# Optimization experiments

Measured on AMD Instinct MI355X. Metric: run time of the kernel, lower is better.

## Reference

```python
import jax, jax.numpy as jnp
import numpy as np

N_EVENTS = 16
N_SAMPLES = 2 ** 15  # 32768


def fft_shift(stems, shift_samples):
    """Fractionally shift each atom in time via frequency-domain phase rotation.
    stems: (B, E, N) float32; shift_samples: (B, E) float32 in [0, N].
    """
    n = stems.shape[-1]
    freqs = jnp.fft.rfftfreq(n).astype(jnp.float32)  # (n//2+1,) cycles/sample
    theta = 2.0 * jnp.pi * freqs[None, None, :] * shift_samples[..., None]  # (B,E,F)
    phase = jnp.cos(theta) - 1j * jnp.sin(theta)  # exp(-i*theta)
    spec = jnp.fft.rfft(stems, axis=-1)
    return jnp.fft.irfft(spec * phase, n=n, axis=-1)


def setup_inputs() -> dict:
    key = jax.random.key(0)
    k1, k2, k3, k4 = jax.random.split(key, 4)
    B = 64
    time_latent = jax.random.normal(k1, (B, N_EVENTS, 128), dtype=jnp.float32)
    stems = jax.random.normal(k2, (B, N_EVENTS, N_SAMPLES), dtype=jnp.float32)
    targets = jax.random.normal(k3, (B, 1, N_SAMPLES), dtype=jnp.float32)
    W_pos = jax.random.normal(k4, (1, 128), dtype=jnp.float32) * 0.1
    b_pos = jnp.zeros((1,), dtype=jnp.float32)
    return {"time_latent": time_latent, "stems": stems, "targets": targets,
            "W_pos": W_pos, "b_pos": b_pos}


def reference(time_latent, stems, targets, W_pos, b_pos):
    # to_pos: Linear(128 -> 1), then sigmoid -> fractional positions in [0,1]
    pos = jax.nn.sigmoid(jnp.einsum('bed,od->beo', time_latent, W_pos) + b_pos)
    pos = pos.reshape(-1, N_EVENTS)  # (B, E)
    # schedule_atoms: place each stem at fractional offset pos * n_samples, sum events
    shifted = fft_shift(stems, pos * N_SAMPLES)  # (B, E, N)
    scheduled = jnp.sum(shifted, axis=1, keepdims=True)  # (B, 1, N), same shape as targets
    return scheduled
```

## Files before the change

### kernel.cpp

```cpp
#include <hip/hip_runtime.h>
#include <math.h>

#define NS      32768
#define M       16384
#define NEV     16
#define NB      64
#define T2      1024

__device__ __forceinline__ int ldsIdx(int i) { return i + (i >> 5) + (i >> 10); }
#define LDS_ELEMS (M + M / 32 + M / 1024)

__device__ __forceinline__ float2 cmul(float2 a, float2 b) {
    return make_float2(a.x * b.x - a.y * b.y, a.x * b.y + a.y * b.x);
}

__device__ __forceinline__ int rev4_14(int i) {
    int r = 0;
#pragma unroll
    for (int d = 0; d < 7; ++d) { r = (r << 2) | (i & 3); i >>= 2; }
    return r;
}

__device__ __forceinline__ float2 shift_phase(int k, int si, float sf) {
    unsigned ksi = ((unsigned)k * (unsigned)si) & (unsigned)(NS - 1);
    float total = (float)ksi + (float)k * sf;
    float f = total * (1.0f / (float)NS);
    f -= floorf(f);
    float ang = -6.28318530717958647692f * f;
    float sv, cv;
    __sincosf(ang, &sv, &cv);
    return make_float2(cv, sv);
}

__device__ __forceinline__ float2 wNS(int k) {
    float ang = (float)k * (-6.28318530717958647692f / (float)NS);
    float sv, cv;
    __sincosf(ang, &sv, &cv);
    return make_float2(cv, sv);
}

__device__ __constant__ float R16C[4] = {1.0f, 0.92387953251128675613f,
                                         0.70710678118654752440f, 0.38268343236508977173f};
__device__ __constant__ float R16S[4] = {0.0f, 0.38268343236508977173f,
                                         0.70710678118654752440f, 0.92387953251128675613f};

__device__ __constant__ float C32[16] = {
    1.0f, 0.98078528040323044913f, 0.92387953251128675613f, 0.83146961230254523708f,
    0.70710678118654752440f, 0.55557023301960222474f, 0.38268343236508977173f,
    0.19509032201612826785f, 0.0f, -0.19509032201612826785f, -0.38268343236508977173f,
    -0.55557023301960222474f, -0.70710678118654752440f, -0.83146961230254523708f,
    -0.92387953251128675613f, -0.98078528040323044913f};
__device__ __constant__ float S32[16] = {
    0.0f, 0.19509032201612826785f, 0.38268343236508977173f, 0.55557023301960222474f,
    0.70710678118654752440f, 0.83146961230254523708f, 0.92387953251128675613f,
    0.98078528040323044913f, 1.0f, 0.98078528040323044913f, 0.92387953251128675613f,
    0.83146961230254523708f, 0.70710678118654752440f, 0.55557023301960222474f,
    0.38268343236508977173f, 0.19509032201612826785f};

template <int SIGN>
__device__ __forceinline__ void btf4(float2* a) {
    float2 a0 = a[0], a1 = a[1], a2 = a[2], a3 = a[3];
    float2 u0 = make_float2(a0.x + a2.x, a0.y + a2.y);
    float2 u1 = make_float2(a0.x - a2.x, a0.y - a2.y);
    float2 u2 = make_float2(a1.x + a3.x, a1.y + a3.y);
    float2 u3 = make_float2(a1.x - a3.x, a1.y - a3.y);
    a[0] = make_float2(u0.x + u2.x, u0.y + u2.y);
    a[2] = make_float2(u0.x - u2.x, u0.y - u2.y);
    if (SIGN < 0) {
        a[1] = make_float2(u1.x + u3.y, u1.y - u3.x);
        a[3] = make_float2(u1.x - u3.y, u1.y + u3.x);
    } else {
        a[1] = make_float2(u1.x - u3.y, u1.y + u3.x);
        a[3] = make_float2(u1.x + u3.y, u1.y - u3.x);
    }
}

template <int SIGN>
__device__ __forceinline__ void load_stage0_scatter(const float4* __restrict__ src,
                                                    float2* lds, int tid) {
    const int R = rev4_14(2 * tid);
    float2 g0[4], g1[4], g2[4], g3[4];
#pragma unroll
    for (int it = 0; it < 8; ++it) {
        float4 v = src[tid + (it << 10)];
        int l = it >> 1;
        if ((it & 1) == 0) { g0[l] = make_float2(v.x, v.y); g1[l] = make_float2(v.z, v.w); }
        else               { g2[l] = make_float2(v.x, v.y); g3[l] = make_float2(v.z, v.w); }
    }
    btf4<SIGN>(g0); btf4<SIGN>(g1); btf4<SIGN>(g2); btf4<SIGN>(g3);
#pragma unroll
    for (int l = 0; l < 4; ++l) {
        lds[ldsIdx(R + l)]               = g0[l];
        lds[ldsIdx(R + 4096 + l)]        = g1[l];
        lds[ldsIdx(R + 8 + l)]           = g2[l];
        lds[ldsIdx(R + 8 + 4096 + l)]    = g3[l];
    }
}

template <int SIGN>
__device__ void fft_pairs(float2* lds, int tid) {
    const float TP = (SIGN < 0) ? -6.28318530717958647692f
                                :  6.28318530717958647692f;
#pragma unroll
    for (int tp = 0; tp < 3; ++tp) {
        const int t = 2 * tp + 1;
        const int q = 1 << (2 * t);
        const int j = tid & (q - 1);
        const int base = ((tid >> (2 * t)) << (2 * t + 4)) + j;
        float2 x[16];
#pragma unroll
        for (int l = 0; l < 16; ++l) x[l] = lds[ldsIdx(base + l * q)];

        float sv, cv;
        __sincosf(TP * (float)j / (float)(16 * q), &sv, &cv);
        float2 ww = make_float2(cv, sv);
        float2 s2 = cmul(ww, ww);
        float2 w1 = cmul(s2, s2);
        float2 w2 = cmul(w1, w1);
        float2 w3 = cmul(w2, w1);

#pragma unroll
        for (int m = 0; m < 4; ++m) {
            float2 a0 = x[4 * m], a1 = x[4 * m + 1], a2 = x[4 * m + 2], a3 = x[4 * m + 3];
            a1 = cmul(a1, w1); a2 = cmul(a2, w2); a3 = cmul(a3, w3);
            float2 u0 = make_float2(a0.x + a2.x, a0.y + a2.y);
            float2 u1 = make_float2(a0.x - a2.x, a0.y - a2.y);
            float2 u2 = make_float2(a1.x + a3.x, a1.y + a3.y);
            float2 u3 = make_float2(a1.x - a3.x, a1.y - a3.y);
            x[4 * m]     = make_float2(u0.x + u2.x, u0.y + u2.y);
            x[4 * m + 2] = make_float2(u0.x - u2.x, u0.y - u2.y);
            if (SIGN < 0) {
                x[4 * m + 1] = make_float2(u1.x + u3.y, u1.y - u3.x);
                x[4 * m + 3] = make_float2(u1.x - u3.y, u1.y + u3.x);
            } else {
                x[4 * m + 1] = make_float2(u1.x - u3.y, u1.y + u3.x);
                x[4 * m + 3] = make_float2(u1.x + u3.y, u1.y - u3.x);
            }
        }

#pragma unroll
        for (int n = 0; n < 4; ++n) {
            float2 a0 = x[n], a1 = x[n + 4], a2 = x[n + 8], a3 = x[n + 12];
            {
                float2 r = make_float2(R16C[n], (SIGN < 0) ? -R16S[n] : R16S[n]);
                float2 wp = (n > 0) ? cmul(ww, r) : ww;
                float2 wp2 = cmul(wp, wp);
                float2 wp3 = cmul(wp2, wp);
                a1 = cmul(a1, wp);
                a2 = cmul(a2, wp2);
                a3 = cmul(a3, wp3);
            }
            float2 u0 = make_float2(a0.x + a2.x, a0.y + a2.y);
            float2 u1 = make_float2(a0.x - a2.x, a0.y - a2.y);
            float2 u2 = make_float2(a1.x + a3.x, a1.y + a3.y);
            float2 u3 = make_float2(a1.x - a3.x, a1.y - a3.y);
            x[n]      = make_float2(u0.x + u2.x, u0.y + u2.y);
            x[n + 8]  = make_float2(u0.x - u2.x, u0.y - u2.y);
            if (SIGN < 0) {
                x[n + 4]  = make_float2(u1.x + u3.y, u1.y - u3.x);
                x[n + 12] = make_float2(u1.x - u3.y, u1.y + u3.x);
            } else {
                x[n + 4]  = make_float2(u1.x - u3.y, u1.y + u3.x);
                x[n + 12] = make_float2(u1.x + u3.y, u1.y - u3.x);
            }
        }
#pragma unroll
        for (int l = 0; l < 16; ++l) lds[ldsIdx(base + l * q)] = x[l];
        __syncthreads();
    }
}

__device__ __forceinline__ void zpair(float2 a, float2 bb, float2 w,
                                      float2* z1, float2* z2) {
    float2 E1 = make_float2(0.5f * (a.x + bb.x), 0.5f * (a.y - bb.y));
    float2 D1 = make_float2(0.5f * (a.x - bb.x), 0.5f * (a.y + bb.y));
    float2 O1 = cmul(make_float2(w.x, -w.y), D1);
    *z1 = make_float2(E1.x - O1.y, E1.y + O1.x);
    float2 D2 = make_float2(-D1.x, D1.y);
    float2 O2p = cmul(w, D2);
    *z2 = make_float2(E1.x + O2p.y, -E1.y - O2p.x);
}

__global__ __launch_bounds__(T2, 4) void fft_phase_kernel(float* __restrict__ stems,
                                                          const float* __restrict__ tl,
                                                          const float* __restrict__ W,
                                                          const float* __restrict__ bp) {
    __shared__ float2 lds[LDS_ELEMS];
    __shared__ float sh_shift;
    const int tid = threadIdx.x;
    const int row = blockIdx.x;
    float* rowp = stems + (size_t)row * NS;

    if (tid < 64) {
        const float* trow = tl + (size_t)row * 128;
        float p = trow[tid] * W[tid] + trow[tid + 64] * W[tid + 64];
#pragma unroll
        for (int off = 32; off > 0; off >>= 1) p += __shfl_down(p, off);
        if (tid == 0) {
            float x = p + bp[0];
            sh_shift = (1.0f / (1.0f + expf(-x))) * (float)NS;
        }
    }

    load_stage0_scatter<-1>((const float4*)rowp, lds, tid);
    __syncthreads();
    fft_pairs<-1>(lds, tid);

    const float s = sh_shift;
    const int si = (int)floorf(s);
    const float sf = s - (float)si;
    float2* spec = (float2*)rowp;

    float msv, mcv;
    __sincosf(-3.14159265358979323846f * sf, &msv, &mcv);
    float2 phM = make_float2(mcv, msv);
    if (si & 1) { phM.x = -phM.x; phM.y = -phM.y; }

    const float2 ph0 = shift_phase(tid, si, sf);
    const float2 w0  = wNS(tid);
    const float2 q1  = shift_phase(1024, si, sf);
    const float2 q2  = cmul(q1, q1);
    const float2 q3  = cmul(q2, q1);
    const float2 q4  = cmul(q2, q2);
    float2 phb = ph0;
#pragma unroll
    for (int t = 0; t < 8; ++t) {
        int k = tid + (t << 10);
        float2 ph;
        switch (t & 3) {
            case 0:  ph = phb; break;
            case 1:  ph = cmul(phb, q1); break;
            case 2:  ph = cmul(phb, q2); break;
            default: ph = cmul(phb, q3); break;
        }
        if (k == 0) {
            float2 z0 = lds[ldsIdx(0)];
            float X0 = z0.x + z0.y;
            float XM = z0.x - z0.y;
            float Nq = XM * phM.x;
            spec[0] = make_float2(0.5f * (X0 + Nq), 0.5f * (X0 - Nq));
            float2 Zh = lds[ldsIdx(M / 2)];
            float2 Xh = make_float2(Zh.x, -Zh.y);
            float2 ph_h = shift_phase(M / 2, si, sf);
            float2 Ah = cmul(Xh, ph_h);
            spec[M / 2] = make_float2(Ah.x, -Ah.y);
        } else {
            float2 Zk = lds[ldsIdx(k)];
            float2 Zr = lds[ldsIdx(M - k)];
            float2 E = make_float2(0.5f * (Zk.x + Zr.x), 0.5f * (Zk.y - Zr.y));
            float2 O = make_float2(0.5f * (Zk.y + Zr.y), -0.5f * (Zk.x - Zr.x));
            float2 w = cmul(w0, make_float2(C32[t], -S32[t]));
            float2 wo = cmul(w, O);
            float2 Xk = make_float2(E.x + wo.x, E.y + wo.y);
            float2 Xm = make_float2(E.x - wo.x, wo.y - E.y);
            float2 Ak = cmul(Xk, ph);
            float2 phm = cmul(phM, make_float2(ph.x, -ph.y));
            float2 Am = cmul(Xm, phm);
            float2 z1, z2;
            zpair(Ak, Am, w, &z1, &z2);
            spec[k] = z1;
            spec[M - k] = z2;
        }
        if ((t & 3) == 3) phb = cmul(phb, q4);
    }
}

__global__ __launch_bounds__(256) void reduce_kernel(const float4* __restrict__ stems,
                                                     float4* __restrict__ out) {
    int gid = blockIdx.x * 256 + threadIdx.x;
    int b = gid >> 13;
    int i = gid & (NS / 4 - 1);
    const float4* base = stems + (size_t)b * NEV * (NS / 4) + i;
    float4 s = base[0];
#pragma unroll
    for (int e = 1; e < NEV; ++e) {
        float4 v = base[(size_t)e * (NS / 4)];
        s.x += v.x; s.y += v.y; s.z += v.z; s.w += v.w;
    }
    out[gid] = s;
}

__global__ __launch_bounds__(T2, 4) void inv_kernel(float* __restrict__ out) {
    __shared__ float2 lds[LDS_ELEMS];
    const int tid = threadIdx.x;
    const int b = blockIdx.x;
    float* rowp = out + (size_t)b * NS;

    load_stage0_scatter<1>((const float4*)rowp, lds, tid);
    __syncthreads();
    fft_pairs<1>(lds, tid);

    const float invM = 1.0f / (float)M;
    float4* dst = (float4*)rowp;
#pragma unroll
    for (int it = 0; it < (NS / 4) / T2; ++it) {
        int i = tid + it * T2;
        float2 z0 = lds[ldsIdx(2 * i)];
        float2 z1 = lds[ldsIdx(2 * i + 1)];
        dst[i] = make_float4(z0.x * invM, z0.y * invM, z1.x * invM, z1.y * invM);
    }
}

extern "C" void kernel_launch(void* const* d_in, const int* in_sizes, int n_in,
                              void* d_out, int out_size, void* d_ws, size_t ws_size,
                              hipStream_t stream) {
    const float* time_latent = (const float*)d_in[0];
    float* stems = (float*)d_in[1];
    const float* W_pos = (const float*)d_in[3];
    const float* b_pos = (const float*)d_in[4];
    float* out = (float*)d_out;

    fft_phase_kernel<<<NB * NEV, T2, 0, stream>>>(stems, time_latent, W_pos, b_pos);
    reduce_kernel<<<(NB * NS / 4) / 256, 256, 0, stream>>>((const float4*)stems,
                                                           (float4*)out);
    inv_kernel<<<NB, T2, 0, stream>>>(out);
}
```

Before: 284.7 us.

## Accumulate four events' shifted spectra per block before writing partials

Each block now runs forward FFTs and phase shifts for four events in sequence and keeps the summed spectrum in registers. It writes one partial spectrum per group of four instead of one per event, and the reduce kernel sums only four partials. This cuts global write and reduce read traffic by four times. In exchange the grid shrinks to a quarter as many blocks, each doing serial work with extra accumulator registers, which may reduce latency hiding. If the workspace is too small it falls back to writing partials into the stems buffer, which could overwrite rows other blocks have not read yet.

```diff
diff --git a/kernel.cpp b/kernel.cpp
--- a/kernel.cpp
+++ b/kernel.cpp
@@ -6,6 +6,8 @@
 #define NEV     16
 #define NB      64
 #define T2      1024
+#define EPB     4
+#define NGRP    (NEV / EPB)
 
 __device__ __forceinline__ int ldsIdx(int i) { return i + (i >> 5) + (i >> 10); }
 #define LDS_ELEMS (M + M / 32 + M / 1024)
@@ -181,100 +183,138 @@
     *z2 = make_float2(E1.x + O2p.y, -E1.y - O2p.x);
 }
 
-__global__ __launch_bounds__(T2, 4) void fft_phase_kernel(float* __restrict__ stems,
-                                                          const float* __restrict__ tl,
-                                                          const float* __restrict__ W,
-                                                          const float* __restrict__ bp) {
+__global__ __launch_bounds__(T2, 4) void fft_phase_acc(const float* __restrict__ stems,
+                                                       float* __restrict__ zpart,
+                                                       const float* __restrict__ tl,
+                                                       const float* __restrict__ W,
+                                                       const float* __restrict__ bp) {
     __shared__ float2 lds[LDS_ELEMS];
-    __shared__ float sh_shift;
+    __shared__ float sh_shift[EPB];
     const int tid = threadIdx.x;
-    const int row = blockIdx.x;
-    float* rowp = stems + (size_t)row * NS;
-
-    if (tid < 64) {
-        const float* trow = tl + (size_t)row * 128;
-        float p = trow[tid] * W[tid] + trow[tid + 64] * W[tid + 64];
+    const int b = blockIdx.x >> 2;
+    const int g = blockIdx.x & 3;
+    const int rowbase = b * NEV + g * EPB;
+
+    if (tid < EPB * 64) {
+        const int w = tid >> 6, lane = tid & 63;
+        const float* trow = tl + (size_t)(rowbase + w) * 128;
+        float p = trow[lane] * W[lane] + trow[lane + 64] * W[lane + 64];
 #pragma unroll
         for (int off = 32; off > 0; off >>= 1) p += __shfl_down(p, off);
-        if (tid == 0) {
+        if (lane == 0) {
             float x = p + bp[0];
-            sh_shift = (1.0f / (1.0f + expf(-x))) * (float)NS;
-        }
-    }
-
-    load_stage0_scatter<-1>((const float4*)rowp, lds, tid);
-    __syncthreads();
-    fft_pairs<-1>(lds, tid);
-
-    const float s = sh_shift;
-    const int si = (int)floorf(s);
-    const float sf = s - (float)si;
-    float2* spec = (float2*)rowp;
-
-    float msv, mcv;
-    __sincosf(-3.14159265358979323846f * sf, &msv, &mcv);
-    float2 phM = make_float2(mcv, msv);
-    if (si & 1) { phM.x = -phM.x; phM.y = -phM.y; }
-
-    const float2 ph0 = shift_phase(tid, si, sf);
-    const float2 w0  = wNS(tid);
-    const float2 q1  = shift_phase(1024, si, sf);
-    const float2 q2  = cmul(q1, q1);
-    const float2 q3  = cmul(q2, q1);
-    const float2 q4  = cmul(q2, q2);
-    float2 phb = ph0;
+            sh_shift[w] = (1.0f / (1.0f + expf(-x))) * (float)NS;
+        }
+    }
+
+    float2 accK[8], accR[8];
+#pragma unroll
+    for (int t = 0; t < 8; ++t) {
+        accK[t] = make_float2(0.f, 0.f);
+        accR[t] = make_float2(0.f, 0.f);
+    }
+    const float2 w0 = wNS(tid);
+
+    for (int ee = 0; ee < EPB; ++ee) {
+        const float* rowp = stems + (size_t)(rowbase + ee) * NS;
+        load_stage0_scatter<-1>((const float4*)rowp, lds, tid);
+        __syncthreads();
+        fft_pairs<-1>(lds, tid);
+
+        const float s = sh_shift[ee];
+        const int si = (int)floorf(s);
+        const float sf = s - (float)si;
+
+        float msv, mcv;
+        __sincosf(-3.14159265358979323846f * sf, &msv, &mcv);
+        float2 phM = make_float2(mcv, msv);
+        if (si & 1) { phM.x = -phM.x; phM.y = -phM.y; }
+
+        const float2 ph0 = shift_phase(tid, si, sf);
+        const float2 q1  = shift_phase(1024, si, sf);
+        const float2 q2  = cmul(q1, q1);
+        const float2 q3  = cmul(q2, q1);
+        const float2 q4  = cmul(q2, q2);
+        float2 phb = ph0;
+#pragma unroll
+        for (int t = 0; t < 8; ++t) {
+            int k = tid + (t << 10);
+            float2 ph;
+            switch (t & 3) {
+                case 0:  ph = phb; break;
+                case 1:  ph = cmul(phb, q1); break;
+                case 2:  ph = cmul(phb, q2); break;
+                default: ph = cmul(phb, q3); break;
+            }
+            if (k == 0) {
+                float2 z0 = lds[ldsIdx(0)];
+                float X0 = z0.x + z0.y;
+                float XM = z0.x - z0.y;
+                float Nq = XM * phM.x;
+                accK[0].x += 0.5f * (X0 + Nq);
+                accK[0].y += 0.5f * (X0 - Nq);
+                float2 Zh = lds[ldsIdx(M / 2)];
+                float2 Xh = make_float2(Zh.x, -Zh.y);
+                float2 ph_h = shift_phase(M / 2, si, sf);
+                float2 Ah = cmul(Xh, ph_h);
+                accR[0].x += Ah.x;
+                accR[0].y += -Ah.y;
+            } else {
+                float2 Zk = lds[ldsIdx(k)];
+                float2 Zr = lds[ldsIdx(M - k)];
+                float2 E = make_float2(0.5f * (Zk.x + Zr.x), 0.5f * (Zk.y - Zr.y));
+                float2 O = make_float2(0.5f * (Zk.y + Zr.y), -0.5f * (Zk.x - Zr.x));
+                float2 w = cmul(w0, make_float2(C32[t], -S32[t]));
+                float2 wo = cmul(w, O);
+                float2 Xk = make_float2(E.x + wo.x, E.y + wo.y);
+                float2 Xm = make_float2(E.x - wo.x, wo.y - E.y);
+                float2 Ak = cmul(Xk, ph);
+                float2 phm = cmul(phM, make_float2(ph.x, -ph.y));
+                float2 Am = cmul(Xm, phm);
+                float2 z1, z2;
+                zpair(Ak, Am, w, &z1, &z2);
+                accK[t].x += z1.x; accK[t].y += z1.y;
+                accR[t].x += z2.x; accR[t].y += z2.y;
+            }
+            if ((t & 3) == 3) phb = cmul(phb, q4);
+        }
+        __syncthreads();
+    }
+
 #pragma unroll
     for (int t = 0; t < 8; ++t) {
         int k = tid + (t << 10);
-        float2 ph;
-        switch (t & 3) {
-            case 0:  ph = phb; break;
-            case 1:  ph = cmul(phb, q1); break;
-            case 2:  ph = cmul(phb, q2); break;
-            default: ph = cmul(phb, q3); break;
-        }
         if (k == 0) {
-            float2 z0 = lds[ldsIdx(0)];
-            float X0 = z0.x + z0.y;
-            float XM = z0.x - z0.y;
-            float Nq = XM * phM.x;
-            spec[0] = make_float2(0.5f * (X0 + Nq), 0.5f * (X0 - Nq));
-            float2 Zh = lds[ldsIdx(M / 2)];
-            float2 Xh = make_float2(Zh.x, -Zh.y);
-            float2 ph_h = shift_phase(M / 2, si, sf);
-            float2 Ah = cmul(Xh, ph_h);
-            spec[M / 2] = make_float2(Ah.x, -Ah.y);
+            lds[ldsIdx(0)]     = accK[0];
+            lds[ldsIdx(M / 2)] = accR[0];
         } else {
-            float2 Zk = lds[ldsIdx(k)];
-            float2 Zr = lds[ldsIdx(M - k)];
-            float2 E = make_float2(0.5f * (Zk.x + Zr.x), 0.5f * (Zk.y - Zr.y));
-            float2 O = make_float2(0.5f * (Zk.y + Zr.y), -0.5f * (Zk.x - Zr.x));
-            float2 w = cmul(w0, make_float2(C32[t], -S32[t]));
-            float2 wo = cmul(w, O);
-            float2 Xk = make_float2(E.x + wo.x, E.y + wo.y);
-            float2 Xm = make_float2(E.x - wo.x, wo.y - E.y);
-            float2 Ak = cmul(Xk, ph);
-            float2 phm = cmul(phM, make_float2(ph.x, -ph.y));
-            float2 Am = cmul(Xm, phm);
-            float2 z1, z2;
-            zpair(Ak, Am, w, &z1, &z2);
-            spec[k] = z1;
-            spec[M - k] = z2;
-        }
-        if ((t & 3) == 3) phb = cmul(phb, q4);
-    }
-}
-
-__global__ __launch_bounds__(256) void reduce_kernel(const float4* __restrict__ stems,
-                                                     float4* __restrict__ out) {
+            lds[ldsIdx(k)]     = accK[t];
+            lds[ldsIdx(M - k)] = accR[t];
+        }
+    }
+    __syncthreads();
+
+    float4* dst = (float4*)(zpart + (size_t)(g * NB + b) * NS);
+#pragma unroll
+    for (int it = 0; it < (NS / 4) / T2; ++it) {
+        int i = tid + it * T2;
+        float2 z0 = lds[ldsIdx(2 * i)];
+        float2 z1 = lds[ldsIdx(2 * i + 1)];
+        dst[i] = make_float4(z0.x, z0.y, z1.x, z1.y);
+    }
+}
+
+__global__ __launch_bounds__(256) void reduce4_kernel(const float4* __restrict__ zpart,
+                                                      float4* __restrict__ out) {
     int gid = blockIdx.x * 256 + threadIdx.x;
     int b = gid >> 13;
     int i = gid & (NS / 4 - 1);
-    const float4* base = stems + (size_t)b * NEV * (NS / 4) + i;
+    const size_t stride = (size_t)NB * (NS / 4);
+    const float4* base = zpart + (size_t)b * (NS / 4) + i;
     float4 s = base[0];
 #pragma unroll
-    for (int e = 1; e < NEV; ++e) {
-        float4 v = base[(size_t)e * (NS / 4)];
+    for (int gr = 1; gr < NGRP; ++gr) {
+        float4 v = base[gr * stride];
         s.x += v.x; s.y += v.y; s.z += v.z; s.w += v.w;
     }
     out[gid] = s;
@@ -310,8 +350,12 @@
     const float* b_pos = (const float*)d_in[4];
     float* out = (float*)d_out;
 
-    fft_phase_kernel<<<NB * NEV, T2, 0, stream>>>(stems, time_latent, W_pos, b_pos);
-    reduce_kernel<<<(NB * NS / 4) / 256, 256, 0, stream>>>((const float4*)stems,
-                                                           (float4*)out);
+    const size_t PBYTES = (size_t)NGRP * NB * NS * sizeof(float);
+    float* zpart = (ws_size >= PBYTES) ? (float*)d_ws : stems;
+
+    fft_phase_acc<<<NB * NGRP, T2, 0, stream>>>(stems, zpart, time_latent,
+                                                W_pos, b_pos);
+    reduce4_kernel<<<(NB * NS / 4) / 256, 256, 0, stream>>>((const float4*)zpart,
+                                                            (float4*)out);
     inv_kernel<<<NB, T2, 0, stream>>>(out);
 }
```

Result: slower. 467.8 us (+64.3%).
